# Optimization experiments

Measured on AMD Instinct MI355X. Metric: run time of the kernel, lower is better.

## Reference

```python
import jax, jax.numpy as jnp
import numpy as np

B, N, C = 8, 1024, 768
H = 12
HD = C // H
RANK = 8
SCALE = HD ** -0.5


def setup_inputs() -> dict:
    key = jax.random.key(0)
    ks = jax.random.split(key, 12)
    s = C ** -0.5
    inp = {
        'x': jax.random.normal(ks[0], (B, N, C), jnp.float32),
        'w_qkv': jax.random.normal(ks[1], (3 * C, C), jnp.float32) * s,
        'b_qkv': jax.random.normal(ks[2], (3 * C,), jnp.float32) * 0.02,
        'w_proj': jax.random.normal(ks[3], (C, C), jnp.float32) * s,
        'b_proj': jax.random.normal(ks[4], (C,), jnp.float32) * 0.02,
        # LoRA A matrices (kaiming-uniform-ish); B matrices are zero at init,
        # but use small nonzero values so the adapter path is exercised.
        'q_a': jax.random.normal(ks[5], (RANK, C), jnp.float32) * s,
        'q_b': jax.random.normal(ks[6], (C, RANK), jnp.float32) * 0.01,
        'k_a': jax.random.normal(ks[7], (RANK, C), jnp.float32) * s,
        'k_b': jax.random.normal(ks[8], (C, RANK), jnp.float32) * 0.01,
        'v_a': jax.random.normal(ks[9], (RANK, C), jnp.float32) * s,
        'v_b': jax.random.normal(ks[10], (C, RANK), jnp.float32) * 0.01,
        'o_a': jax.random.normal(ks[11], (RANK, C), jnp.float32) * s,
        'o_b': jax.random.normal(jax.random.fold_in(key, 99), (C, RANK), jnp.float32) * 0.01,
    }
    return inp


def _lora(x, wa, wb):
    # x:[B,N,C], wa:[r,C], wb:[C,r] -> [B,N,C]
    return jnp.einsum('bnr,cr->bnc', jnp.einsum('bnc,rc->bnr', x, wa), wb)


def reference(x, w_qkv, b_qkv, w_proj, b_proj, q_a, q_b, k_a, k_b, v_a, v_b, o_a, o_b):
    # QKV projection + fused LoRA slice-adds
    qkv = jnp.einsum('bnc,dc->bnd', x, w_qkv) + b_qkv  # [B,N,3C]
    q = qkv[:, :, :C] + _lora(x, q_a, q_b)
    k = qkv[:, :, C:2 * C] + _lora(x, k_a, k_b)
    v = qkv[:, :, 2 * C:] + _lora(x, v_a, v_b)
    # [B,H,N,HD]
    q = q.reshape(B, N, H, HD).transpose(0, 2, 1, 3)
    k = k.reshape(B, N, H, HD).transpose(0, 2, 1, 3)
    v = v.reshape(B, N, H, HD).transpose(0, 2, 1, 3)
    attn = jnp.einsum('bhqd,bhkd->bhqk', q, k) * SCALE
    attn = jax.nn.softmax(attn, axis=-1)  # dropout is identity in eval
    o = jnp.einsum('bhqk,bhkd->bhqd', attn, v)
    o = o.transpose(0, 2, 1, 3).reshape(B, N, C)
    out = jnp.einsum('bnc,dc->bnd', o, w_proj) + b_proj + _lora(o, o_a, o_b)
    return out
```

## Files before the change

### kernel.cpp

```cpp
#include <hip/hip_runtime.h>

typedef __attribute__((ext_vector_type(8))) short short8;
typedef __attribute__((ext_vector_type(4))) float f32x4;
typedef __attribute__((ext_vector_type(4))) unsigned short u16x4;
typedef __attribute__((ext_vector_type(2))) unsigned int u32x2;

#define MFMA16(a,b,c) __builtin_amdgcn_mfma_f32_16x16x32_bf16((a),(b),(c),0,0,0)

#define QSCALE 0.1803368801f

__device__ __forceinline__ unsigned short f2bf(float f) {
  unsigned int x = __float_as_uint(f);
  x += 0x7fffu + ((x >> 16) & 1u);
  return (unsigned short)(x >> 16);
}
__device__ __forceinline__ unsigned int pack2bf(float a, float b) {
  unsigned int ua = __float_as_uint(a) + 0x8000u;
  unsigned int ub = __float_as_uint(b) + 0x8000u;
  return __builtin_amdgcn_perm(ub, ua, 0x07060302);
}

__global__ __launch_bounds__(256) void convert_x(
    const float* __restrict__ x, unsigned short* __restrict__ xb)
{
  int i4 = (blockIdx.x * 256 + threadIdx.x) * 4;
  f32x4 v = *(const f32x4*)&x[i4];
  u16x4 o;
  o.x = f2bf(v.x); o.y = f2bf(v.y); o.z = f2bf(v.z); o.w = f2bf(v.w);
  *(u16x4*)&xb[i4] = o;
}

__global__ __launch_bounds__(256) void build_weights(
    const float* __restrict__ w_qkv,
    const float* __restrict__ w_proj,
    const float* __restrict__ q_a, const float* __restrict__ q_b,
    const float* __restrict__ k_a, const float* __restrict__ k_b,
    const float* __restrict__ v_a, const float* __restrict__ v_b,
    const float* __restrict__ o_a, const float* __restrict__ o_b,
    unsigned short* __restrict__ wqkv_eff,
    unsigned short* __restrict__ wproj_eff)
{
  const int QKV = 2304 * 768;
  int idx = blockIdx.x * 256 + threadIdx.x;
  if (idx < QKV) {
    int n = idx / 768, c = idx - n * 768;
    int sec = n / 768;
    int nr = n - sec * 768;
    const float* a; const float* b;
    if (sec == 0)      { a = q_a; b = q_b; }
    else if (sec == 1) { a = k_a; b = k_b; }
    else               { a = v_a; b = v_b; }
    float acc = w_qkv[idx];
    #pragma unroll
    for (int r = 0; r < 8; r++)
      acc += b[nr * 8 + r] * a[r * 768 + c];
    wqkv_eff[idx] = f2bf(acc);
  } else {
    int i2 = idx - QKV;
    int n = i2 / 768, c = i2 - n * 768;
    float acc = w_proj[i2];
    #pragma unroll
    for (int r = 0; r < 8; r++)
      acc += o_b[n * 8 + r] * o_a[r * 768 + c];
    wproj_eff[i2] = f2bf(acc);
  }
}

__global__ __launch_bounds__(256) void gemm_bt(
    const unsigned short* __restrict__ A,
    const unsigned short* __restrict__ W,
    const float* __restrict__ bias,
    unsigned short* __restrict__ out0,
    unsigned short* __restrict__ out1,
    unsigned short* __restrict__ out2,
    float* __restrict__ outf,
    int K, int Ncols, int mode)
{
  __shared__ alignas(16) unsigned short As[128][72];
  __shared__ alignas(16) unsigned short Ws[64][72];
  const int tid  = threadIdx.x;
  const int wave = tid >> 6;
  const int lane = tid & 63;
  const int quad = lane >> 4;
  const int l16  = lane & 15;
  const int m0 = blockIdx.x * 128;
  const int n0 = blockIdx.y * 64;

  int ar[4], ac[4], wr[2], wc[2];
  #pragma unroll
  for (int i = 0; i < 4; i++) { int f = tid + i * 256; ar[i] = f >> 3; ac[i] = (f & 7) << 3; }
  #pragma unroll
  for (int i = 0; i < 2; i++) { int f = tid + i * 256; wr[i] = f >> 3; wc[i] = (f & 7) << 3; }

  f32x4 areg[4], wreg[2];
  #pragma unroll
  for (int i = 0; i < 4; i++)
    areg[i] = *(const f32x4*)&A[(size_t)(m0 + ar[i]) * K + ac[i]];
  #pragma unroll
  for (int i = 0; i < 2; i++)
    wreg[i] = *(const f32x4*)&W[(size_t)(n0 + wr[i]) * K + wc[i]];

  f32x4 acc[2][4] = {};

  for (int k0 = 0; k0 < K; k0 += 64) {
    __syncthreads();
    #pragma unroll
    for (int i = 0; i < 4; i++) *(f32x4*)&As[ar[i]][ac[i]] = areg[i];
    #pragma unroll
    for (int i = 0; i < 2; i++) *(f32x4*)&Ws[wr[i]][wc[i]] = wreg[i];
    __syncthreads();
    if (k0 + 64 < K) {
      #pragma unroll
      for (int i = 0; i < 4; i++)
        areg[i] = *(const f32x4*)&A[(size_t)(m0 + ar[i]) * K + k0 + 64 + ac[i]];
      #pragma unroll
      for (int i = 0; i < 2; i++)
        wreg[i] = *(const f32x4*)&W[(size_t)(n0 + wr[i]) * K + k0 + 64 + wc[i]];
    }
    #pragma unroll
    for (int ks = 0; ks < 2; ks++) {
      const int kk = ks * 32 + quad * 8;
      short8 a0 = *(const short8*)&As[wave * 32 + l16][kk];
      short8 a1 = *(const short8*)&As[wave * 32 + 16 + l16][kk];
      short8 b0 = *(const short8*)&Ws[l16][kk];
      short8 b1 = *(const short8*)&Ws[16 + l16][kk];
      short8 b2 = *(const short8*)&Ws[32 + l16][kk];
      short8 b3 = *(const short8*)&Ws[48 + l16][kk];
      acc[0][0] = MFMA16(a0, b0, acc[0][0]);
      acc[0][1] = MFMA16(a0, b1, acc[0][1]);
      acc[0][2] = MFMA16(a0, b2, acc[0][2]);
      acc[0][3] = MFMA16(a0, b3, acc[0][3]);
      acc[1][0] = MFMA16(a1, b0, acc[1][0]);
      acc[1][1] = MFMA16(a1, b1, acc[1][1]);
      acc[1][2] = MFMA16(a1, b2, acc[1][2]);
      acc[1][3] = MFMA16(a1, b3, acc[1][3]);
    }
  }

  float bv[4];
  #pragma unroll
  for (int j = 0; j < 4; j++) bv[j] = bias[n0 + j * 16 + l16];

  if (mode == 0) {
    const int sec = n0 / 768;
    const int h   = (n0 % 768) >> 6;
    unsigned short* dst = (sec == 0) ? out0 : ((sec == 1) ? out1 : out2);
    const float scl = (sec == 0) ? QSCALE : 1.0f;
    #pragma unroll
    for (int rg = 0; rg < 2; rg++) {
      #pragma unroll
      for (int r = 0; r < 4; r++) {
        int m  = m0 + wave * 32 + rg * 16 + quad * 4 + r;
        int b  = m >> 10, np = m & 1023;
        int bh = b * 12 + h;
        int npp = (np & ~63) | ((np & 15) * 4 + ((np >> 4) & 3));
        #pragma unroll
        for (int j = 0; j < 4; j++) {
          int d = j * 16 + l16;
          float v = (acc[rg][j][r] + bv[j]) * scl;
          if (sec < 2) dst[((size_t)bh << 16) + ((size_t)np << 6) + d] = f2bf(v);
          else         dst[((size_t)bh << 16) + ((size_t)d << 10) + npp] = f2bf(v);
        }
      }
    }
  } else {
    #pragma unroll
    for (int rg = 0; rg < 2; rg++) {
      #pragma unroll
      for (int r = 0; r < 4; r++) {
        int m = m0 + wave * 32 + rg * 16 + quad * 4 + r;
        #pragma unroll
        for (int j = 0; j < 4; j++)
          outf[(size_t)m * Ncols + n0 + j * 16 + l16] = acc[rg][j][r] + bv[j];
      }
    }
  }
}

__global__ __launch_bounds__(256) void attn(
    const unsigned short* __restrict__ q,
    const unsigned short* __restrict__ k,
    const unsigned short* __restrict__ vt,
    unsigned short* __restrict__ o)
{
  __shared__ alignas(16) unsigned short Qs[128][72];
  __shared__ alignas(16) unsigned short Ks[64][72];
  __shared__ alignas(16) unsigned short Vs[64][72];
  const int tid  = threadIdx.x;
  const int wave = tid >> 6;
  const int lane = tid & 63;
  const int quad = lane >> 4;
  const int l16  = lane & 15;
  const int bh = blockIdx.x;
  const int q0 = blockIdx.y * 128;
  const unsigned short* qb = q  + ((size_t)bh << 16);
  const unsigned short* kb = k  + ((size_t)bh << 16);
  const unsigned short* vb = vt + ((size_t)bh << 16);

  #pragma unroll
  for (int i = 0; i < 4; i++) {
    int flat = tid + i * 256;
    int r = flat >> 3, ck = (flat & 7) << 3;
    *(f32x4*)&Qs[r][ck] = *(const f32x4*)&qb[((size_t)(q0 + r) << 6) + ck];
  }
  __syncthreads();
  short8 aq[2][2];
  #pragma unroll
  for (int rg = 0; rg < 2; rg++)
    #pragma unroll
    for (int ks = 0; ks < 2; ks++)
      aq[rg][ks] = *(const short8*)&Qs[wave * 32 + rg * 16 + l16][ks * 32 + quad * 8];
  __syncthreads();
  unsigned short (*Ps)[72] = (unsigned short (*)[72])(&Qs[wave * 32][0]);

  f32x4 Oacc[2][4] = {};
  float lsum[2][4] = {};

  int sr[2], sc[2];
  #pragma unroll
  for (int i = 0; i < 2; i++) { int f = tid + i * 256; sr[i] = f >> 3; sc[i] = (f & 7) << 3; }

  f32x4 kreg[2], vreg[2];
  #pragma unroll
  for (int i = 0; i < 2; i++) {
    kreg[i] = *(const f32x4*)&kb[((size_t)sr[i] << 6) + sc[i]];
    vreg[i] = *(const f32x4*)&vb[((size_t)sr[i] << 10) + sc[i]];
  }

  for (int kt = 0; kt < 16; kt++) {
    __syncthreads();
    #pragma unroll
    for (int i = 0; i < 2; i++) {
      *(f32x4*)&Ks[sr[i]][sc[i]] = kreg[i];
      *(f32x4*)&Vs[sr[i]][sc[i]] = vreg[i];
    }
    __syncthreads();
    if (kt < 15) {
      #pragma unroll
      for (int i = 0; i < 2; i++) {
        kreg[i] = *(const f32x4*)&kb[((size_t)((kt + 1) * 64 + sr[i]) << 6) + sc[i]];
        vreg[i] = *(const f32x4*)&vb[((size_t)sr[i] << 10) + (kt + 1) * 64 + sc[i]];
      }
    }

    f32x4 s[2][4] = {};
    #pragma unroll
    for (int ks = 0; ks < 2; ks++) {
      const int kk = ks * 32 + quad * 8;
      short8 b0 = *(const short8*)&Ks[l16][kk];
      short8 b1 = *(const short8*)&Ks[16 + l16][kk];
      short8 b2 = *(const short8*)&Ks[32 + l16][kk];
      short8 b3 = *(const short8*)&Ks[48 + l16][kk];
      s[0][0] = MFMA16(aq[0][ks], b0, s[0][0]);
      s[0][1] = MFMA16(aq[0][ks], b1, s[0][1]);
      s[0][2] = MFMA16(aq[0][ks], b2, s[0][2]);
      s[0][3] = MFMA16(aq[0][ks], b3, s[0][3]);
      s[1][0] = MFMA16(aq[1][ks], b0, s[1][0]);
      s[1][1] = MFMA16(aq[1][ks], b1, s[1][1]);
      s[1][2] = MFMA16(aq[1][ks], b2, s[1][2]);
      s[1][3] = MFMA16(aq[1][ks], b3, s[1][3]);
    }

    #pragma unroll
    for (int rg = 0; rg < 2; rg++) {
      #pragma unroll
      for (int r = 0; r < 4; r++) {
        float p0 = exp2f(s[rg][0][r]);
        float p1 = exp2f(s[rg][1][r]);
        float p2 = exp2f(s[rg][2][r]);
        float p3 = exp2f(s[rg][3][r]);
        lsum[rg][r] += (p0 + p1) + (p2 + p3);
        u32x2 pk;
        pk.x = pack2bf(p0, p1);
        pk.y = pack2bf(p2, p3);
        *(u32x2*)&Ps[rg * 16 + quad * 4 + r][4 * l16] = pk;
      }
    }

    #pragma unroll
    for (int ks = 0; ks < 2; ks++) {
      const int kk = ks * 32 + quad * 8;
      short8 a0 = *(const short8*)&Ps[l16][kk];
      short8 a1 = *(const short8*)&Ps[16 + l16][kk];
      short8 v0 = *(const short8*)&Vs[l16][kk];
      short8 v1 = *(const short8*)&Vs[16 + l16][kk];
      short8 v2 = *(const short8*)&Vs[32 + l16][kk];
      short8 v3 = *(const short8*)&Vs[48 + l16][kk];
      Oacc[0][0] = MFMA16(a0, v0, Oacc[0][0]);
      Oacc[0][1] = MFMA16(a0, v1, Oacc[0][1]);
      Oacc[0][2] = MFMA16(a0, v2, Oacc[0][2]);
      Oacc[0][3] = MFMA16(a0, v3, Oacc[0][3]);
      Oacc[1][0] = MFMA16(a1, v0, Oacc[1][0]);
      Oacc[1][1] = MFMA16(a1, v1, Oacc[1][1]);
      Oacc[1][2] = MFMA16(a1, v2, Oacc[1][2]);
      Oacc[1][3] = MFMA16(a1, v3, Oacc[1][3]);
    }
  }

  const int b = bh / 12, h = bh - (bh / 12) * 12;
  #pragma unroll
  for (int rg = 0; rg < 2; rg++) {
    #pragma unroll
    for (int r = 0; r < 4; r++) {
      float t = lsum[rg][r];
      t += __shfl_xor(t, 1, 64);
      t += __shfl_xor(t, 2, 64);
      t += __shfl_xor(t, 4, 64);
      t += __shfl_xor(t, 8, 64);
      float inv = 1.0f / t;
      int np = q0 + wave * 32 + rg * 16 + quad * 4 + r;
      size_t base = ((size_t)(b * 1024 + np)) * 768 + h * 64;
      #pragma unroll
      for (int j = 0; j < 4; j++)
        o[base + j * 16 + l16] = f2bf(Oacc[rg][j][r] * inv);
    }
  }
}

extern "C" void kernel_launch(void* const* d_in, const int* in_sizes, int n_in,
                              void* d_out, int out_size, void* d_ws, size_t ws_size,
                              hipStream_t stream) {
  const float* x      = (const float*)d_in[0];
  const float* w_qkv  = (const float*)d_in[1];
  const float* b_qkv  = (const float*)d_in[2];
  const float* w_proj = (const float*)d_in[3];
  const float* b_proj = (const float*)d_in[4];
  const float* q_a    = (const float*)d_in[5];
  const float* q_b    = (const float*)d_in[6];
  const float* k_a    = (const float*)d_in[7];
  const float* k_b    = (const float*)d_in[8];
  const float* v_a    = (const float*)d_in[9];
  const float* v_b    = (const float*)d_in[10];
  const float* o_a    = (const float*)d_in[11];
  const float* o_b    = (const float*)d_in[12];

  char* ws = (char*)d_ws;
  unsigned short* wqkv_eff  = (unsigned short*)(ws + 0);
  unsigned short* wproj_eff = (unsigned short*)(ws + 3538944);
  unsigned short* xb        = (unsigned short*)(ws + 4718592);
  unsigned short* qd        = (unsigned short*)(ws + 17301504);
  unsigned short* kd        = (unsigned short*)(ws + 29884416);
  unsigned short* vtd       = (unsigned short*)(ws + 42467328);
  unsigned short* od        = xb;

  convert_x<<<dim3(6144), dim3(256), 0, stream>>>(x, xb);

  build_weights<<<dim3(9216), dim3(256), 0, stream>>>(
      w_qkv, w_proj, q_a, q_b, k_a, k_b, v_a, v_b, o_a, o_b, wqkv_eff, wproj_eff);

  gemm_bt<<<dim3(64, 36), dim3(256), 0, stream>>>(
      xb, wqkv_eff, b_qkv, qd, kd, vtd, nullptr, 768, 2304, 0);

  attn<<<dim3(96, 8), dim3(256), 0, stream>>>(qd, kd, vtd, od);

  gemm_bt<<<dim3(64, 12), dim3(256), 0, stream>>>(
      od, wproj_eff, b_proj, nullptr, nullptr, nullptr, (float*)d_out, 768, 768, 1);
}
```

Baseline: 225.4 us.

## Enlarge GEMM tiles to 128x128 with direct global-to-LDS loads and fuse prep kernels

Merges the x conversion and the weight-folding kernels into one launch. Reworks the GEMM to 128x128 tiles with a 2x2 wave layout (4x4 MFMA accumulators per wave). Tiles are loaded with global_load_lds straight into XOR-swizzled, unpadded shared memory. The aim is more operand reuse per LDS read, fewer launches, and less register staging. The cost is that register prefetch overlap is gone: loads are issued at the top of each iteration and the kernel syncs before compute, so there is no double buffering. The projection GEMM now launches only 384 blocks, which may underfill the GPU.

```diff
diff --git a/kernel.cpp b/kernel.cpp
--- a/kernel.cpp
+++ b/kernel.cpp
@@ -19,29 +19,35 @@
   unsigned int ub = __float_as_uint(b) + 0x8000u;
   return __builtin_amdgcn_perm(ub, ua, 0x07060302);
 }
-
-__global__ __launch_bounds__(256) void convert_x(
-    const float* __restrict__ x, unsigned short* __restrict__ xb)
-{
-  int i4 = (blockIdx.x * 256 + threadIdx.x) * 4;
-  f32x4 v = *(const f32x4*)&x[i4];
-  u16x4 o;
-  o.x = f2bf(v.x); o.y = f2bf(v.y); o.z = f2bf(v.z); o.w = f2bf(v.w);
-  *(u16x4*)&xb[i4] = o;
-}
-
-__global__ __launch_bounds__(256) void build_weights(
+__device__ __forceinline__ void gload16(const unsigned short* g, unsigned short* l) {
+  __builtin_amdgcn_global_load_lds(
+      (const __attribute__((address_space(1))) unsigned int*)g,
+      (__attribute__((address_space(3))) unsigned int*)l, 16, 0, 0);
+}
+
+__global__ __launch_bounds__(256) void prep(
+    const float* __restrict__ x,
     const float* __restrict__ w_qkv,
     const float* __restrict__ w_proj,
     const float* __restrict__ q_a, const float* __restrict__ q_b,
     const float* __restrict__ k_a, const float* __restrict__ k_b,
     const float* __restrict__ v_a, const float* __restrict__ v_b,
     const float* __restrict__ o_a, const float* __restrict__ o_b,
+    unsigned short* __restrict__ xb,
     unsigned short* __restrict__ wqkv_eff,
     unsigned short* __restrict__ wproj_eff)
 {
+  int bid = blockIdx.x;
+  if (bid < 6144) {
+    int i4 = (bid * 256 + threadIdx.x) * 4;
+    f32x4 v = *(const f32x4*)&x[i4];
+    u16x4 o;
+    o.x = f2bf(v.x); o.y = f2bf(v.y); o.z = f2bf(v.z); o.w = f2bf(v.w);
+    *(u16x4*)&xb[i4] = o;
+    return;
+  }
   const int QKV = 2304 * 768;
-  int idx = blockIdx.x * 256 + threadIdx.x;
+  int idx = (bid - 6144) * 256 + threadIdx.x;
   if (idx < QKV) {
     int n = idx / 768, c = idx - n * 768;
     int sec = n / 768;
@@ -76,88 +82,81 @@
     float* __restrict__ outf,
     int K, int Ncols, int mode)
 {
-  __shared__ alignas(16) unsigned short As[128][72];
-  __shared__ alignas(16) unsigned short Ws[64][72];
+  __shared__ alignas(16) unsigned short As[128 * 64];
+  __shared__ alignas(16) unsigned short Ws[128 * 64];
   const int tid  = threadIdx.x;
   const int wave = tid >> 6;
   const int lane = tid & 63;
   const int quad = lane >> 4;
   const int l16  = lane & 15;
+  const int wr   = wave >> 1, wc = wave & 1;
   const int m0 = blockIdx.x * 128;
-  const int n0 = blockIdx.y * 64;
-
-  int ar[4], ac[4], wr[2], wc[2];
-  #pragma unroll
-  for (int i = 0; i < 4; i++) { int f = tid + i * 256; ar[i] = f >> 3; ac[i] = (f & 7) << 3; }
-  #pragma unroll
-  for (int i = 0; i < 2; i++) { int f = tid + i * 256; wr[i] = f >> 3; wc[i] = (f & 7) << 3; }
-
-  f32x4 areg[4], wreg[2];
-  #pragma unroll
-  for (int i = 0; i < 4; i++)
-    areg[i] = *(const f32x4*)&A[(size_t)(m0 + ar[i]) * K + ac[i]];
-  #pragma unroll
-  for (int i = 0; i < 2; i++)
-    wreg[i] = *(const f32x4*)&W[(size_t)(n0 + wr[i]) * K + wc[i]];
-
-  f32x4 acc[2][4] = {};
+  const int n0 = blockIdx.y * 128;
+
+  const int lrow   = lane >> 3;
+  const int lchunk = (lane & 7) ^ lrow;
+  const unsigned short* gA[4];
+  const unsigned short* gW[4];
+  unsigned short* lA[4];
+  unsigned short* lW[4];
+  #pragma unroll
+  for (int t = 0; t < 4; t++) {
+    int rr = wave * 32 + t * 8;
+    gA[t] = A + (size_t)(m0 + rr + lrow) * K + lchunk * 8;
+    gW[t] = W + (size_t)(n0 + rr + lrow) * K + lchunk * 8;
+    lA[t] = &As[(rr + lrow) * 64 + (lane & 7) * 8];
+    lW[t] = &Ws[(rr + lrow) * 64 + (lane & 7) * 8];
+  }
+
+  f32x4 acc[4][4] = {};
+  const int swz = (l16 & 7);
 
   for (int k0 = 0; k0 < K; k0 += 64) {
+    #pragma unroll
+    for (int t = 0; t < 4; t++) {
+      gload16(gA[t] + k0, lA[t]);
+      gload16(gW[t] + k0, lW[t]);
+    }
     __syncthreads();
     #pragma unroll
-    for (int i = 0; i < 4; i++) *(f32x4*)&As[ar[i]][ac[i]] = areg[i];
-    #pragma unroll
-    for (int i = 0; i < 2; i++) *(f32x4*)&Ws[wr[i]][wc[i]] = wreg[i];
+    for (int ks = 0; ks < 2; ks++) {
+      const int cs = ks * 4 + quad;
+      short8 a[4], b[4];
+      #pragma unroll
+      for (int t = 0; t < 4; t++) {
+        a[t] = *(const short8*)&As[(wr * 64 + t * 16 + l16) * 64 + ((cs ^ swz) << 3)];
+        b[t] = *(const short8*)&Ws[(wc * 64 + t * 16 + l16) * 64 + ((cs ^ swz) << 3)];
+      }
+      #pragma unroll
+      for (int i = 0; i < 4; i++)
+        #pragma unroll
+        for (int j = 0; j < 4; j++)
+          acc[i][j] = MFMA16(a[i], b[j], acc[i][j]);
+    }
     __syncthreads();
-    if (k0 + 64 < K) {
-      #pragma unroll
-      for (int i = 0; i < 4; i++)
-        areg[i] = *(const f32x4*)&A[(size_t)(m0 + ar[i]) * K + k0 + 64 + ac[i]];
-      #pragma unroll
-      for (int i = 0; i < 2; i++)
-        wreg[i] = *(const f32x4*)&W[(size_t)(n0 + wr[i]) * K + k0 + 64 + wc[i]];
-    }
-    #pragma unroll
-    for (int ks = 0; ks < 2; ks++) {
-      const int kk = ks * 32 + quad * 8;
-      short8 a0 = *(const short8*)&As[wave * 32 + l16][kk];
-      short8 a1 = *(const short8*)&As[wave * 32 + 16 + l16][kk];
-      short8 b0 = *(const short8*)&Ws[l16][kk];
-      short8 b1 = *(const short8*)&Ws[16 + l16][kk];
-      short8 b2 = *(const short8*)&Ws[32 + l16][kk];
-      short8 b3 = *(const short8*)&Ws[48 + l16][kk];
-      acc[0][0] = MFMA16(a0, b0, acc[0][0]);
-      acc[0][1] = MFMA16(a0, b1, acc[0][1]);
-      acc[0][2] = MFMA16(a0, b2, acc[0][2]);
-      acc[0][3] = MFMA16(a0, b3, acc[0][3]);
-      acc[1][0] = MFMA16(a1, b0, acc[1][0]);
-      acc[1][1] = MFMA16(a1, b1, acc[1][1]);
-      acc[1][2] = MFMA16(a1, b2, acc[1][2]);
-      acc[1][3] = MFMA16(a1, b3, acc[1][3]);
-    }
   }
 
   float bv[4];
   #pragma unroll
-  for (int j = 0; j < 4; j++) bv[j] = bias[n0 + j * 16 + l16];
+  for (int j = 0; j < 4; j++) bv[j] = bias[n0 + wc * 64 + j * 16 + l16];
 
   if (mode == 0) {
     const int sec = n0 / 768;
-    const int h   = (n0 % 768) >> 6;
+    const int h   = ((n0 % 768) >> 6) + wc;
     unsigned short* dst = (sec == 0) ? out0 : ((sec == 1) ? out1 : out2);
     const float scl = (sec == 0) ? QSCALE : 1.0f;
     #pragma unroll
-    for (int rg = 0; rg < 2; rg++) {
+    for (int i = 0; i < 4; i++) {
       #pragma unroll
       for (int r = 0; r < 4; r++) {
-        int m  = m0 + wave * 32 + rg * 16 + quad * 4 + r;
-        int b  = m >> 10, np = m & 1023;
-        int bh = b * 12 + h;
+        int m  = m0 + wr * 64 + i * 16 + quad * 4 + r;
+        int bb = m >> 10, np = m & 1023;
+        int bh = bb * 12 + h;
         int npp = (np & ~63) | ((np & 15) * 4 + ((np >> 4) & 3));
         #pragma unroll
         for (int j = 0; j < 4; j++) {
           int d = j * 16 + l16;
-          float v = (acc[rg][j][r] + bv[j]) * scl;
+          float v = (acc[i][j][r] + bv[j]) * scl;
           if (sec < 2) dst[((size_t)bh << 16) + ((size_t)np << 6) + d] = f2bf(v);
           else         dst[((size_t)bh << 16) + ((size_t)d << 10) + npp] = f2bf(v);
         }
@@ -165,13 +164,13 @@
     }
   } else {
     #pragma unroll
-    for (int rg = 0; rg < 2; rg++) {
+    for (int i = 0; i < 4; i++) {
       #pragma unroll
       for (int r = 0; r < 4; r++) {
-        int m = m0 + wave * 32 + rg * 16 + quad * 4 + r;
+        int m = m0 + wr * 64 + i * 16 + quad * 4 + r;
         #pragma unroll
         for (int j = 0; j < 4; j++)
-          outf[(size_t)m * Ncols + n0 + j * 16 + l16] = acc[rg][j][r] + bv[j];
+          outf[(size_t)m * Ncols + n0 + wc * 64 + j * 16 + l16] = acc[i][j][r] + bv[j];
       }
     }
   }
@@ -343,16 +342,15 @@
   unsigned short* vtd       = (unsigned short*)(ws + 42467328);
   unsigned short* od        = xb;
 
-  convert_x<<<dim3(6144), dim3(256), 0, stream>>>(x, xb);
-
-  build_weights<<<dim3(9216), dim3(256), 0, stream>>>(
-      w_qkv, w_proj, q_a, q_b, k_a, k_b, v_a, v_b, o_a, o_b, wqkv_eff, wproj_eff);
-
-  gemm_bt<<<dim3(64, 36), dim3(256), 0, stream>>>(
+  prep<<<dim3(6144 + 9216), dim3(256), 0, stream>>>(
+      x, w_qkv, w_proj, q_a, q_b, k_a, k_b, v_a, v_b, o_a, o_b,
+      xb, wqkv_eff, wproj_eff);
+
+  gemm_bt<<<dim3(64, 18), dim3(256), 0, stream>>>(
       xb, wqkv_eff, b_qkv, qd, kd, vtd, nullptr, 768, 2304, 0);
 
   attn<<<dim3(96, 8), dim3(256), 0, stream>>>(qd, kd, vtd, od);
 
-  gemm_bt<<<dim3(64, 12), dim3(256), 0, stream>>>(
+  gemm_bt<<<dim3(64, 6), dim3(256), 0, stream>>>(
       od, wproj_eff, b_proj, nullptr, nullptr, nullptr, (float*)d_out, 768, 768, 1);
 }
```

New measurement: 224.0 us. About the same (-0.6%).

## Double-buffer attention K/V via direct global-to-LDS loads with XOR swizzle

Applied to the files above, without the earlier changes.

The attention kernel now stages K and V tiles straight from global memory into two LDS buffers with global_load_lds, prefetching the next tile while the current one is consumed. The old path loaded through registers and wrote them back to shared memory. The shared tiles drop the padded rows and use an XOR chunk swizzle to avoid bank conflicts, and one barrier is removed from each iteration. Separately, the x-conversion and weight-building kernels are merged into one launch to save launch overhead. The change relies on the async LDS writes being complete before the barrier, which adds a risk to correctness if the needed waits are not inserted.

```diff
diff --git a/kernel.cpp b/kernel.cpp
--- a/kernel.cpp
+++ b/kernel.cpp
@@ -19,29 +19,35 @@
   unsigned int ub = __float_as_uint(b) + 0x8000u;
   return __builtin_amdgcn_perm(ub, ua, 0x07060302);
 }
-
-__global__ __launch_bounds__(256) void convert_x(
-    const float* __restrict__ x, unsigned short* __restrict__ xb)
-{
-  int i4 = (blockIdx.x * 256 + threadIdx.x) * 4;
-  f32x4 v = *(const f32x4*)&x[i4];
-  u16x4 o;
-  o.x = f2bf(v.x); o.y = f2bf(v.y); o.z = f2bf(v.z); o.w = f2bf(v.w);
-  *(u16x4*)&xb[i4] = o;
-}
-
-__global__ __launch_bounds__(256) void build_weights(
+__device__ __forceinline__ void gload16(const unsigned short* g, unsigned short* l) {
+  __builtin_amdgcn_global_load_lds(
+      (const __attribute__((address_space(1))) unsigned int*)g,
+      (__attribute__((address_space(3))) unsigned int*)l, 16, 0, 0);
+}
+
+__global__ __launch_bounds__(256) void prep(
+    const float* __restrict__ x,
     const float* __restrict__ w_qkv,
     const float* __restrict__ w_proj,
     const float* __restrict__ q_a, const float* __restrict__ q_b,
     const float* __restrict__ k_a, const float* __restrict__ k_b,
     const float* __restrict__ v_a, const float* __restrict__ v_b,
     const float* __restrict__ o_a, const float* __restrict__ o_b,
+    unsigned short* __restrict__ xb,
     unsigned short* __restrict__ wqkv_eff,
     unsigned short* __restrict__ wproj_eff)
 {
+  int bid = blockIdx.x;
+  if (bid < 6144) {
+    int i4 = (bid * 256 + threadIdx.x) * 4;
+    f32x4 v = *(const f32x4*)&x[i4];
+    u16x4 o;
+    o.x = f2bf(v.x); o.y = f2bf(v.y); o.z = f2bf(v.z); o.w = f2bf(v.w);
+    *(u16x4*)&xb[i4] = o;
+    return;
+  }
   const int QKV = 2304 * 768;
-  int idx = blockIdx.x * 256 + threadIdx.x;
+  int idx = (bid - 6144) * 256 + threadIdx.x;
   if (idx < QKV) {
     int n = idx / 768, c = idx - n * 768;
     int sec = n / 768;
@@ -184,8 +190,8 @@
     unsigned short* __restrict__ o)
 {
   __shared__ alignas(16) unsigned short Qs[128][72];
-  __shared__ alignas(16) unsigned short Ks[64][72];
-  __shared__ alignas(16) unsigned short Vs[64][72];
+  __shared__ alignas(16) unsigned short Ks2[2][64 * 64];
+  __shared__ alignas(16) unsigned short Vs2[2][64 * 64];
   const int tid  = threadIdx.x;
   const int wave = tid >> 6;
   const int lane = tid & 63;
@@ -197,6 +203,26 @@
   const unsigned short* kb = k  + ((size_t)bh << 16);
   const unsigned short* vb = vt + ((size_t)bh << 16);
 
+  const int lrow   = lane >> 3;
+  const int lchunk = (lane & 7) ^ lrow;
+  const unsigned short* gK[2];
+  const unsigned short* gV[2];
+  int lsKV[2];
+  #pragma unroll
+  for (int t = 0; t < 2; t++) {
+    int rr = wave * 16 + t * 8 + lrow;
+    gK[t]   = kb + (size_t)rr * 64 + lchunk * 8;
+    gV[t]   = vb + (size_t)rr * 1024 + lchunk * 8;
+    lsKV[t] = rr * 64 + (lane & 7) * 8;
+  }
+  const int swz = l16 & 7;
+
+  #pragma unroll
+  for (int t = 0; t < 2; t++) {
+    gload16(gK[t], &Ks2[0][lsKV[t]]);
+    gload16(gV[t], &Vs2[0][lsKV[t]]);
+  }
+
   #pragma unroll
   for (int i = 0; i < 4; i++) {
     int flat = tid + i * 256;
@@ -210,47 +236,30 @@
     #pragma unroll
     for (int ks = 0; ks < 2; ks++)
       aq[rg][ks] = *(const short8*)&Qs[wave * 32 + rg * 16 + l16][ks * 32 + quad * 8];
-  __syncthreads();
   unsigned short (*Ps)[72] = (unsigned short (*)[72])(&Qs[wave * 32][0]);
 
   f32x4 Oacc[2][4] = {};
   float lsum[2][4] = {};
 
-  int sr[2], sc[2];
-  #pragma unroll
-  for (int i = 0; i < 2; i++) { int f = tid + i * 256; sr[i] = f >> 3; sc[i] = (f & 7) << 3; }
-
-  f32x4 kreg[2], vreg[2];
-  #pragma unroll
-  for (int i = 0; i < 2; i++) {
-    kreg[i] = *(const f32x4*)&kb[((size_t)sr[i] << 6) + sc[i]];
-    vreg[i] = *(const f32x4*)&vb[((size_t)sr[i] << 10) + sc[i]];
-  }
-
   for (int kt = 0; kt < 16; kt++) {
-    __syncthreads();
-    #pragma unroll
-    for (int i = 0; i < 2; i++) {
-      *(f32x4*)&Ks[sr[i]][sc[i]] = kreg[i];
-      *(f32x4*)&Vs[sr[i]][sc[i]] = vreg[i];
-    }
+    const int p = kt & 1;
     __syncthreads();
     if (kt < 15) {
       #pragma unroll
-      for (int i = 0; i < 2; i++) {
-        kreg[i] = *(const f32x4*)&kb[((size_t)((kt + 1) * 64 + sr[i]) << 6) + sc[i]];
-        vreg[i] = *(const f32x4*)&vb[((size_t)sr[i] << 10) + (kt + 1) * 64 + sc[i]];
+      for (int t = 0; t < 2; t++) {
+        gload16(gK[t] + (kt + 1) * 4096, &Ks2[1 - p][lsKV[t]]);
+        gload16(gV[t] + (kt + 1) * 64,   &Vs2[1 - p][lsKV[t]]);
       }
     }
 
     f32x4 s[2][4] = {};
     #pragma unroll
     for (int ks = 0; ks < 2; ks++) {
-      const int kk = ks * 32 + quad * 8;
-      short8 b0 = *(const short8*)&Ks[l16][kk];
-      short8 b1 = *(const short8*)&Ks[16 + l16][kk];
-      short8 b2 = *(const short8*)&Ks[32 + l16][kk];
-      short8 b3 = *(const short8*)&Ks[48 + l16][kk];
+      const int cs = ks * 4 + quad;
+      short8 b0 = *(const short8*)&Ks2[p][(l16)      * 64 + ((cs ^ swz) << 3)];
+      short8 b1 = *(const short8*)&Ks2[p][(16 + l16) * 64 + ((cs ^ swz) << 3)];
+      short8 b2 = *(const short8*)&Ks2[p][(32 + l16) * 64 + ((cs ^ swz) << 3)];
+      short8 b3 = *(const short8*)&Ks2[p][(48 + l16) * 64 + ((cs ^ swz) << 3)];
       s[0][0] = MFMA16(aq[0][ks], b0, s[0][0]);
       s[0][1] = MFMA16(aq[0][ks], b1, s[0][1]);
       s[0][2] = MFMA16(aq[0][ks], b2, s[0][2]);
@@ -280,12 +289,13 @@
     #pragma unroll
     for (int ks = 0; ks < 2; ks++) {
       const int kk = ks * 32 + quad * 8;
+      const int cs = ks * 4 + quad;
       short8 a0 = *(const short8*)&Ps[l16][kk];
       short8 a1 = *(const short8*)&Ps[16 + l16][kk];
-      short8 v0 = *(const short8*)&Vs[l16][kk];
-      short8 v1 = *(const short8*)&Vs[16 + l16][kk];
-      short8 v2 = *(const short8*)&Vs[32 + l16][kk];
-      short8 v3 = *(const short8*)&Vs[48 + l16][kk];
+      short8 v0 = *(const short8*)&Vs2[p][(l16)      * 64 + ((cs ^ swz) << 3)];
+      short8 v1 = *(const short8*)&Vs2[p][(16 + l16) * 64 + ((cs ^ swz) << 3)];
+      short8 v2 = *(const short8*)&Vs2[p][(32 + l16) * 64 + ((cs ^ swz) << 3)];
+      short8 v3 = *(const short8*)&Vs2[p][(48 + l16) * 64 + ((cs ^ swz) << 3)];
       Oacc[0][0] = MFMA16(a0, v0, Oacc[0][0]);
       Oacc[0][1] = MFMA16(a0, v1, Oacc[0][1]);
       Oacc[0][2] = MFMA16(a0, v2, Oacc[0][2]);
@@ -343,10 +353,9 @@
   unsigned short* vtd       = (unsigned short*)(ws + 42467328);
   unsigned short* od        = xb;
 
-  convert_x<<<dim3(6144), dim3(256), 0, stream>>>(x, xb);
-
-  build_weights<<<dim3(9216), dim3(256), 0, stream>>>(
-      w_qkv, w_proj, q_a, q_b, k_a, k_b, v_a, v_b, o_a, o_b, wqkv_eff, wproj_eff);
+  prep<<<dim3(6144 + 9216), dim3(256), 0, stream>>>(
+      x, w_qkv, w_proj, q_a, q_b, k_a, k_b, v_a, v_b, o_a, o_b,
+      xb, wqkv_eff, wproj_eff);
 
   gemm_bt<<<dim3(64, 36), dim3(256), 0, stream>>>(
       xb, wqkv_eff, b_qkv, qd, kd, vtd, nullptr, 768, 2304, 0);
```

After: 226.3 us. About the same (+0.4%).
